# Performance work log

Measured on AMD Instinct MI355X. Metric: run time of the kernel, lower is better.

## Reference

```python
import jax, jax.numpy as jnp
import numpy as np

D = 12            # number of features
N = 1024          # batch size
S = 2 ** D - 1    # number of nonempty subsets (bitmasks 1..2^D-1)
K = 32            # k_neighbors
C = 10            # num_classes
TEMP = 0.5        # temperature
LN_EPS = 1e-5


def _inclusion_matrix():
    # incl[A, B] = 1 if subset B is contained in subset A (bitmask test)
    m = np.arange(1, 2 ** D, dtype=np.int64)
    return ((m[:, None] & m[None, :]) == m[None, :]).astype(np.float32)  # [S, S]

_INCL = _inclusion_matrix()


def setup_inputs() -> dict:
    key = jax.random.key(0)
    ks = jax.random.split(key, 16)
    def g(k, shape, scale):
        return jax.random.normal(k, shape, dtype=jnp.float32) * scale
    return {
        "X": jax.random.normal(ks[0], (N, D), dtype=jnp.float32),
        "y": jax.random.randint(ks[1], (N,), 0, C),
        "enc_w1": g(ks[2], (32, D), 0.3),
        "enc_b1": jnp.zeros((32,), jnp.float32),
        "enc_w2": g(ks[3], (16, 32), 0.2),
        "enc_b2": jnp.zeros((16,), jnp.float32),
        "ln_g": jnp.ones((16,), jnp.float32),
        "ln_b": jnp.zeros((16,), jnp.float32),
        "enc_w3": g(ks[4], (16, 16), 0.25),
        "enc_b3": jnp.zeros((16,), jnp.float32),
        "cap_w1": g(ks[5], (16, 16), 0.1),   # xavier-ish gain=0.1
        "cap_b1": jnp.zeros((16,), jnp.float32),
        "cap_w2": g(ks[6], (S, 16), 0.02),
        "cap_b2": jnp.zeros((S,), jnp.float32),
    }


def _forward(X, y, enc_w1, enc_b1, enc_w2, enc_b2, ln_g, ln_b, enc_w3, enc_b3,
             cap_w1, cap_b1, cap_w2, cap_b2):
    # --- FeatureEncoder (dropout = identity at eval) ---
    h = jax.nn.relu(X @ enc_w1.T + enc_b1)            # [N, 32]
    h = jax.nn.relu(h @ enc_w2.T + enc_b2)            # [N, 16]
    mu = jnp.mean(h, axis=-1, keepdims=True)
    var = jnp.mean((h - mu) ** 2, axis=-1, keepdims=True)
    h = (h - mu) * jax.lax.rsqrt(var + LN_EPS) * ln_g + ln_b
    h = h @ enc_w3.T + enc_b3                         # [N, 16]
    latent = jnp.mean(h, axis=0)                      # [16]

    # --- CapacityGenerator ---
    hc = jax.nn.relu(latent @ cap_w1.T + cap_b1)      # [16]
    increments = jax.nn.sigmoid(hc @ cap_w2.T + cap_b2) * 0.1  # [S]

    # --- compute_capacities_improved: monotone capacities normalized to mu(full)=1 ---
    incl = jnp.asarray(_INCL)                         # [S, S]
    caps = incl @ increments                          # [S]
    caps = caps / (caps[-1] + 1e-8)                   # full set is bitmask 2^D-1 (last)
    cap_lookup = jnp.concatenate([jnp.zeros((1,), caps.dtype), caps])  # index by bitmask, mu(empty)=0

    # --- choquet_similarity_batch for all pairs ---
    s = jnp.exp(-jnp.abs(X[:, None, :] - X[None, :, :]))  # [N, N, D] per-feature sims in (0,1]
    order = jnp.argsort(s, axis=-1)                        # ascending
    vals = jnp.take_along_axis(s, order, axis=-1)          # [N, N, D]
    powers = jnp.left_shift(jnp.int32(1), order.astype(jnp.int32))
    tail = jnp.cumsum(powers[..., ::-1], axis=-1)[..., ::-1]  # bitmask of {sigma(j..D-1)}
    cap = cap_lookup[tail]                                 # [N, N, D]
    prev = jnp.concatenate([jnp.zeros_like(vals[..., :1]), vals[..., :-1]], axis=-1)
    sims = jnp.sum((vals - prev) * cap, axis=-1)           # [N, N] Choquet integral

    # --- leave-one-out top-k softmax vote ---
    sims = sims - jnp.eye(N, dtype=sims.dtype) * 1e9       # exclude self
    top_sims, top_idx = jax.lax.top_k(sims, K)             # [N, K]
    weights = jax.nn.softmax(top_sims / TEMP, axis=-1)     # [N, K]
    labels_k = y[top_idx]                                  # [N, K]
    votes = jnp.einsum('nk,nkc->nc', weights, jax.nn.one_hot(labels_k, C, dtype=weights.dtype))
    return votes, caps


def reference(X, y, enc_w1, enc_b1, enc_w2, enc_b2, ln_g, ln_b, enc_w3, enc_b3,
              cap_w1, cap_b1, cap_w2, cap_b2):
    return _forward(X, y, enc_w1, enc_b1, enc_w2, enc_b2, ln_g, ln_b, enc_w3, enc_b3,
                    cap_w1, cap_b1, cap_w2, cap_b2)
```

## Files before the change

kernel.cpp:

```cpp
#include <hip/hip_runtime.h>

#define ND 12
#define NN 1024
#define NS 4095
#define NK 32
#define NC 10


__global__ __launch_bounds__(64) void k_enc(
    const float* __restrict__ X,
    const float* __restrict__ w1, const float* __restrict__ b1,
    const float* __restrict__ w2, const float* __restrict__ b2,
    const float* __restrict__ lng, const float* __restrict__ lnb,
    const float* __restrict__ w3, const float* __restrict__ b3,
    float* __restrict__ part)
{
    int lane = threadIdx.x;
    int row  = blockIdx.x * 64 + lane;

    float x[ND];
    #pragma unroll
    for (int d = 0; d < ND; ++d) x[d] = X[row * ND + d];

    float h1[32];
    #pragma unroll
    for (int o = 0; o < 32; ++o) {
        float a = b1[o];
        #pragma unroll
        for (int d = 0; d < ND; ++d) a += w1[o * ND + d] * x[d];
        h1[o] = fmaxf(a, 0.f);
    }

    float h2[16];
    #pragma unroll
    for (int o = 0; o < 16; ++o) {
        float a = b2[o];
        #pragma unroll
        for (int k = 0; k < 32; ++k) a += w2[o * 32 + k] * h1[k];
        h2[o] = fmaxf(a, 0.f);
    }

    float mu = 0.f;
    #pragma unroll
    for (int o = 0; o < 16; ++o) mu += h2[o];
    mu *= (1.f / 16.f);
    float var = 0.f;
    #pragma unroll
    for (int o = 0; o < 16; ++o) { float t = h2[o] - mu; var += t * t; }
    var *= (1.f / 16.f);
    float inv = 1.f / sqrtf(var + 1e-5f);

    float hn[16];
    #pragma unroll
    for (int o = 0; o < 16; ++o) hn[o] = (h2[o] - mu) * inv * lng[o] + lnb[o];

    #pragma unroll
    for (int o = 0; o < 16; ++o) {
        float a = b3[o];
        #pragma unroll
        for (int k = 0; k < 16; ++k) a += w3[o * 16 + k] * hn[k];
        #pragma unroll
        for (int s = 1; s < 64; s <<= 1) a += __shfl_xor(a, s, 64);
        if (lane == 0) part[blockIdx.x * 16 + o] = a;
    }
}

__global__ __launch_bounds__(256) void k_inc(
    const float* __restrict__ part,
    const float* __restrict__ cw1, const float* __restrict__ cb1,
    const float* __restrict__ cw2, const float* __restrict__ cb2,
    float* __restrict__ inc)
{
    __shared__ float lat_s[16];
    __shared__ float hc_s[16];
    int tid = threadIdx.x;

    if (tid < 16) {
        float a = 0.f;
        #pragma unroll
        for (int b = 0; b < 16; ++b) a += part[b * 16 + tid];
        lat_s[tid] = a * (1.f / 1024.f);
    }
    __syncthreads();
    if (tid < 16) {
        float a = cb1[tid];
        #pragma unroll
        for (int k = 0; k < 16; ++k) a += cw1[tid * 16 + k] * lat_s[k];
        hc_s[tid] = fmaxf(a, 0.f);
    }
    __syncthreads();

    int e = blockIdx.x * 1024 + tid * 4;
    int s = e >> 4;
    if (s < NS) {
        float4 w = *reinterpret_cast<const float4*>(cw2 + e);
        int k0 = e & 15;
        float p = w.x * hc_s[k0] + w.y * hc_s[k0 + 1] + w.z * hc_s[k0 + 2] + w.w * hc_s[k0 + 3];
        p += __shfl_xor(p, 1, 64);
        p += __shfl_xor(p, 2, 64);
        if ((tid & 3) == 0) {
            float a = p + cb2[s];
            inc[s + 1] = 0.1f / (1.f + __expf(-a));
        }
    }
    if (blockIdx.x == 0 && tid == 0) inc[0] = 0.f;
}

__global__ __launch_bounds__(1024) void k_zeta(
    const float* __restrict__ inc, float* __restrict__ cap_ws, float* __restrict__ out)
{
    __shared__ float arr[4096];
    int tid = threadIdx.x;

    *reinterpret_cast<float4*>(arr + tid * 4) = *reinterpret_cast<const float4*>(inc + tid * 4);
    __syncthreads();

    #pragma unroll 1
    for (int d = 0; d < ND; ++d) {
        int bit = 1 << d;
        #pragma unroll
        for (int r = 0; r < 2; ++r) {
            int i   = tid + r * 1024;
            int low = i & (bit - 1);
            int m   = ((i >> d) << (d + 1)) | bit | low;
            arr[m] += arr[m ^ bit];
        }
        __syncthreads();
    }

    float inv = 1.f / (arr[4095] + 1e-8f);
    #pragma unroll
    for (int r = 0; r < 4; ++r) {
        int m = tid * 4 + r;
        cap_ws[m] = arr[m];
        if (m >= 1) out[NN * NC + m - 1] = arr[m] * inv;
    }
}

#define CSWAP(a,b) { float va=v[a], vb=v[b]; bool sw = va > vb; \
                     v[a]=sw?vb:va; v[b]=sw?va:vb; \
                     int ba=bm[a], bb=bm[b]; bm[a]=sw?bb:ba; bm[b]=sw?ba:bb; }

__global__ __launch_bounds__(256) void k_simsel(
    const float* __restrict__ X, const int* __restrict__ y,
    const float* __restrict__ cap_ws, float* __restrict__ out)
{
    __shared__ float    cap[4096];
    __shared__ unsigned bins[2048];
    __shared__ unsigned wt_u[4];
    __shared__ unsigned ctl_bin, ctl_need;
    __shared__ unsigned vmax_u[4];
    __shared__ float    wsum_s[4];
    __shared__ float    fbins[NC];

    int tid = threadIdx.x, i = blockIdx.x;
    int wv = tid >> 6, ln = tid & 63;

    #pragma unroll
    for (int t = 0; t < 16; ++t) cap[tid + 256 * t] = cap_ws[tid + 256 * t];

    float xi[ND];
    #pragma unroll
    for (int d = 0; d < ND; ++d) xi[d] = X[i * ND + d];
    float inv = 1.f / (cap_ws[4095] + 1e-8f);
    __syncthreads();

    unsigned long long kreg[4];
    #pragma unroll
    for (int t = 0; t < 4; ++t) {
        int j = t * 256 + tid;
        float v[ND]; int bm[ND];
        #pragma unroll
        for (int d = 0; d < ND; ++d) {
            v[d]  = __expf(-fabsf(xi[d] - X[j * ND + d]));
            bm[d] = 1 << d;
        }
        CSWAP(0,1)  CSWAP(0,2)  CSWAP(1,2)  CSWAP(3,4)  CSWAP(3,5)  CSWAP(4,5)
        CSWAP(0,3)  CSWAP(2,5)  CSWAP(2,3)  CSWAP(1,4)  CSWAP(1,2)  CSWAP(3,4)
        CSWAP(6,7)  CSWAP(6,8)  CSWAP(7,8)  CSWAP(9,10) CSWAP(9,11) CSWAP(10,11)
        CSWAP(6,9)  CSWAP(8,11) CSWAP(8,9)  CSWAP(7,10) CSWAP(7,8)  CSWAP(9,10)
        CSWAP(0,6)  CSWAP(4,10) CSWAP(4,6)  CSWAP(2,8)  CSWAP(2,4)  CSWAP(6,8)
        CSWAP(1,7)  CSWAP(5,11) CSWAP(5,7)  CSWAP(3,9)  CSWAP(3,5)  CSWAP(7,9)
        CSWAP(1,2)  CSWAP(3,4)  CSWAP(5,6)  CSWAP(7,8)  CSWAP(9,10)

        int tail = 0; float sim = 0.f;
        #pragma unroll
        for (int k = ND - 1; k >= 0; --k) {
            tail |= bm[k];
            float pv = (k > 0) ? v[k - 1] : 0.f;
            sim += (v[k] - pv) * cap[tail];
        }
        sim *= inv;

        unsigned u = __float_as_uint(sim);
        u = (u & 0x80000000u) ? ~u : (u | 0x80000000u);
        if (j == i) u = 0u;
        kreg[t] = (((unsigned long long)u) << 10) | (unsigned)(1023 - j);
    }

    unsigned mv = 0;
    #pragma unroll
    for (int t = 0; t < 4; ++t) {
        unsigned x = (unsigned)(kreg[t] >> 10);
        mv = (x > mv) ? x : mv;
    }
    #pragma unroll
    for (int s = 1; s < 64; s <<= 1) {
        unsigned o = __shfl_xor(mv, s, 64);
        mv = (o > mv) ? o : mv;
    }
    if (ln == 0) vmax_u[wv] = mv;

    unsigned long long prefix = 0;
    unsigned need = NK;
    #pragma unroll 1
    for (int lev = 0; lev < 4; ++lev) {
        int shift   = (lev < 3) ? (31 - 11 * lev) : 0;
        int bits    = (lev < 3) ? 11 : 9;
        int topbits = shift + bits;
        unsigned mask = (1u << bits) - 1u;

        #pragma unroll
        for (int r = 0; r < 8; ++r) bins[tid + 256 * r] = 0u;
        __syncthreads();

        #pragma unroll
        for (int t = 0; t < 4; ++t) {
            unsigned long long k = kreg[t];
            if ((k >> topbits) == prefix)
                atomicAdd(&bins[(unsigned)(k >> shift) & mask], 1u);
        }
        __syncthreads();

        unsigned s8[8]; unsigned S = 0;
        int base = tid * 8;
        #pragma unroll
        for (int r = 0; r < 8; ++r) { s8[r] = bins[base + r]; S += s8[r]; }
        unsigned v = S;
        #pragma unroll
        for (int off = 1; off < 64; off <<= 1) {
            unsigned o = __shfl_down(v, off, 64);
            if (ln + off < 64) v += o;
        }
        if (ln == 0) wt_u[wv] = v;
        __syncthreads();
        unsigned G = v - S;
        #pragma unroll
        for (int w2 = 0; w2 < 4; ++w2) if (w2 > wv) G += wt_u[w2];

        unsigned cum = G;
        #pragma unroll
        for (int r = 7; r >= 0; --r) {
            unsigned c = s8[r];
            if (cum < need && cum + c >= need) { ctl_bin = (unsigned)(base + r); ctl_need = need - cum; }
            cum += c;
        }
        __syncthreads();
        prefix = (prefix << bits) | ctl_bin;
        need   = ctl_need;
        __syncthreads();
    }
    unsigned long long T = prefix;

    unsigned m0 = vmax_u[0], m1 = vmax_u[1], m2 = vmax_u[2], m3 = vmax_u[3];
    mv = (m1 > m0) ? m1 : m0;
    mv = (m2 > mv) ? m2 : mv;
    mv = (m3 > mv) ? m3 : mv;
    float vmax = (mv & 0x80000000u) ? __uint_as_float(mv & 0x7fffffffu) : __uint_as_float(~mv);

    float wr[4]; float wpart = 0.f;
    #pragma unroll
    for (int t = 0; t < 4; ++t) {
        bool sel = kreg[t] >= T;
        unsigned su = (unsigned)(kreg[t] >> 10);
        float val = (su & 0x80000000u) ? __uint_as_float(su & 0x7fffffffu) : __uint_as_float(~su);
        float w = __expf((val - vmax) * 2.0f);
        w = sel ? w : 0.f;
        wr[t] = w; wpart += w;
    }
    #pragma unroll
    for (int s = 1; s < 64; s <<= 1) wpart += __shfl_xor(wpart, s, 64);
    if (ln == 0) wsum_s[wv] = wpart;
    if (tid < NC) fbins[tid] = 0.f;
    __syncthreads();
    float wsum = wsum_s[0] + wsum_s[1] + wsum_s[2] + wsum_s[3];
    #pragma unroll
    for (int t = 0; t < 4; ++t)
        if (wr[t] != 0.f) atomicAdd(&fbins[y[t * 256 + tid]], wr[t]);
    __syncthreads();
    if (tid < NC) out[i * NC + tid] = fbins[tid] / wsum;
}

extern "C" void kernel_launch(void* const* d_in, const int* in_sizes, int n_in,
                              void* d_out, int out_size, void* d_ws, size_t ws_size,
                              hipStream_t stream)
{
    const float* X   = (const float*)d_in[0];
    const int*   y   = (const int*)  d_in[1];
    const float* w1  = (const float*)d_in[2];
    const float* b1  = (const float*)d_in[3];
    const float* w2  = (const float*)d_in[4];
    const float* b2  = (const float*)d_in[5];
    const float* lng = (const float*)d_in[6];
    const float* lnb = (const float*)d_in[7];
    const float* w3  = (const float*)d_in[8];
    const float* b3  = (const float*)d_in[9];
    const float* cw1 = (const float*)d_in[10];
    const float* cb1 = (const float*)d_in[11];
    const float* cw2 = (const float*)d_in[12];
    const float* cb2 = (const float*)d_in[13];
    float* out = (float*)d_out;
    float* ws  = (float*)d_ws;

    float* cap_ws = ws;
    float* part   = ws + 4096;
    float* inc    = ws + 8192;

    k_enc   <<<16,   64,   0, stream>>>(X, w1, b1, w2, b2, lng, lnb, w3, b3, part);
    k_inc   <<<64,   256,  0, stream>>>(part, cw1, cb1, cw2, cb2, inc);
    k_zeta  <<<1,    1024, 0, stream>>>(inc, cap_ws, out);
    k_simsel<<<NN,   256,  0, stream>>>(X, y, cap_ws, out);
}
```

Baseline: 126.6 us.

## Fuse encoder, capacity generator and zeta transform into one single-block kernel

Merges the three small prep kernels (encoder, increment generator, subset-sum zeta transform) into one 512-thread single-block kernel that keeps partial sums and increments in shared memory, removing two launches and the global round-trips through workspace. The simsel kernel also switches to float4 loads for the cap table, its own row of X and neighbour rows, and clears the histogram bins with uint4 stores. In exchange, the encoder and increment work now run in a single block instead of spread across 16 and 64 blocks, which may lengthen that serial stage.

```diff
diff --git a/kernel.cpp b/kernel.cpp
--- a/kernel.cpp
+++ b/kernel.cpp
@@ -7,78 +7,85 @@
 #define NC 10
 
 
-__global__ __launch_bounds__(64) void k_enc(
+__global__ __launch_bounds__(512) void k_prep(
     const float* __restrict__ X,
     const float* __restrict__ w1, const float* __restrict__ b1,
     const float* __restrict__ w2, const float* __restrict__ b2,
     const float* __restrict__ lng, const float* __restrict__ lnb,
     const float* __restrict__ w3, const float* __restrict__ b3,
-    float* __restrict__ part)
-{
-    int lane = threadIdx.x;
-    int row  = blockIdx.x * 64 + lane;
-
-    float x[ND];
-    #pragma unroll
-    for (int d = 0; d < ND; ++d) x[d] = X[row * ND + d];
-
-    float h1[32];
-    #pragma unroll
-    for (int o = 0; o < 32; ++o) {
-        float a = b1[o];
-        #pragma unroll
-        for (int d = 0; d < ND; ++d) a += w1[o * ND + d] * x[d];
-        h1[o] = fmaxf(a, 0.f);
-    }
-
-    float h2[16];
-    #pragma unroll
-    for (int o = 0; o < 16; ++o) {
-        float a = b2[o];
-        #pragma unroll
-        for (int k = 0; k < 32; ++k) a += w2[o * 32 + k] * h1[k];
-        h2[o] = fmaxf(a, 0.f);
-    }
-
-    float mu = 0.f;
-    #pragma unroll
-    for (int o = 0; o < 16; ++o) mu += h2[o];
-    mu *= (1.f / 16.f);
-    float var = 0.f;
-    #pragma unroll
-    for (int o = 0; o < 16; ++o) { float t = h2[o] - mu; var += t * t; }
-    var *= (1.f / 16.f);
-    float inv = 1.f / sqrtf(var + 1e-5f);
-
-    float hn[16];
-    #pragma unroll
-    for (int o = 0; o < 16; ++o) hn[o] = (h2[o] - mu) * inv * lng[o] + lnb[o];
-
-    #pragma unroll
-    for (int o = 0; o < 16; ++o) {
-        float a = b3[o];
-        #pragma unroll
-        for (int k = 0; k < 16; ++k) a += w3[o * 16 + k] * hn[k];
-        #pragma unroll
-        for (int s = 1; s < 64; s <<= 1) a += __shfl_xor(a, s, 64);
-        if (lane == 0) part[blockIdx.x * 16 + o] = a;
-    }
-}
-
-__global__ __launch_bounds__(256) void k_inc(
-    const float* __restrict__ part,
     const float* __restrict__ cw1, const float* __restrict__ cb1,
     const float* __restrict__ cw2, const float* __restrict__ cb2,
-    float* __restrict__ inc)
+    float* __restrict__ cap_ws, float* __restrict__ out)
 {
+    __shared__ float arr[4096];
+    __shared__ float part[8 * 16];
     __shared__ float lat_s[16];
     __shared__ float hc_s[16];
+
     int tid = threadIdx.x;
+    int wv = tid >> 6, ln = tid & 63;
+
+    float acc[16];
+    #pragma unroll
+    for (int o = 0; o < 16; ++o) acc[o] = 0.f;
+
+    #pragma unroll 1
+    for (int rep = 0; rep < 2; ++rep) {
+        int row = rep * 512 + tid;
+        float x[ND];
+        #pragma unroll
+        for (int d = 0; d < ND; ++d) x[d] = X[row * ND + d];
+
+        float h1[32];
+        #pragma unroll
+        for (int o = 0; o < 32; ++o) {
+            float a = b1[o];
+            #pragma unroll
+            for (int d = 0; d < ND; ++d) a += w1[o * ND + d] * x[d];
+            h1[o] = fmaxf(a, 0.f);
+        }
+        float h2[16];
+        #pragma unroll
+        for (int o = 0; o < 16; ++o) {
+            float a = b2[o];
+            #pragma unroll
+            for (int k = 0; k < 32; ++k) a += w2[o * 32 + k] * h1[k];
+            h2[o] = fmaxf(a, 0.f);
+        }
+        float mu = 0.f;
+        #pragma unroll
+        for (int o = 0; o < 16; ++o) mu += h2[o];
+        mu *= (1.f / 16.f);
+        float var = 0.f;
+        #pragma unroll
+        for (int o = 0; o < 16; ++o) { float t = h2[o] - mu; var += t * t; }
+        var *= (1.f / 16.f);
+        float inv = 1.f / sqrtf(var + 1e-5f);
+        float hn[16];
+        #pragma unroll
+        for (int o = 0; o < 16; ++o) hn[o] = (h2[o] - mu) * inv * lng[o] + lnb[o];
+        #pragma unroll
+        for (int o = 0; o < 16; ++o) {
+            float a = b3[o];
+            #pragma unroll
+            for (int k = 0; k < 16; ++k) a += w3[o * 16 + k] * hn[k];
+            acc[o] += a;
+        }
+    }
+
+    #pragma unroll
+    for (int o = 0; o < 16; ++o) {
+        float a = acc[o];
+        #pragma unroll
+        for (int s = 1; s < 64; s <<= 1) a += __shfl_xor(a, s, 64);
+        if (ln == 0) part[wv * 16 + o] = a;
+    }
+    __syncthreads();
 
     if (tid < 16) {
         float a = 0.f;
         #pragma unroll
-        for (int b = 0; b < 16; ++b) a += part[b * 16 + tid];
+        for (int w = 0; w < 8; ++w) a += part[w * 16 + tid];
         lat_s[tid] = a * (1.f / 1024.f);
     }
     __syncthreads();
@@ -90,37 +97,33 @@
     }
     __syncthreads();
 
-    int e = blockIdx.x * 1024 + tid * 4;
-    int s = e >> 4;
-    if (s < NS) {
-        float4 w = *reinterpret_cast<const float4*>(cw2 + e);
-        int k0 = e & 15;
-        float p = w.x * hc_s[k0] + w.y * hc_s[k0 + 1] + w.z * hc_s[k0 + 2] + w.w * hc_s[k0 + 3];
-        p += __shfl_xor(p, 1, 64);
-        p += __shfl_xor(p, 2, 64);
-        if ((tid & 3) == 0) {
-            float a = p + cb2[s];
-            inc[s + 1] = 0.1f / (1.f + __expf(-a));
-        }
-    }
-    if (blockIdx.x == 0 && tid == 0) inc[0] = 0.f;
-}
-
-__global__ __launch_bounds__(1024) void k_zeta(
-    const float* __restrict__ inc, float* __restrict__ cap_ws, float* __restrict__ out)
-{
-    __shared__ float arr[4096];
-    int tid = threadIdx.x;
-
-    *reinterpret_cast<float4*>(arr + tid * 4) = *reinterpret_cast<const float4*>(inc + tid * 4);
+    float hc[16];
+    #pragma unroll
+    for (int k = 0; k < 16; ++k) hc[k] = hc_s[k];
+    const float4* cw24 = reinterpret_cast<const float4*>(cw2);
+    #pragma unroll 1
+    for (int r = 0; r < 8; ++r) {
+        int s = tid + r * 512;
+        if (s < NS) {
+            float4 wa = cw24[s * 4 + 0], wb = cw24[s * 4 + 1];
+            float4 wc = cw24[s * 4 + 2], wd = cw24[s * 4 + 3];
+            float a = cb2[s]
+                + wa.x * hc[0]  + wa.y * hc[1]  + wa.z * hc[2]  + wa.w * hc[3]
+                + wb.x * hc[4]  + wb.y * hc[5]  + wb.z * hc[6]  + wb.w * hc[7]
+                + wc.x * hc[8]  + wc.y * hc[9]  + wc.z * hc[10] + wc.w * hc[11]
+                + wd.x * hc[12] + wd.y * hc[13] + wd.z * hc[14] + wd.w * hc[15];
+            arr[s + 1] = 0.1f / (1.f + __expf(-a));
+        }
+    }
+    if (tid == 0) arr[0] = 0.f;
     __syncthreads();
 
     #pragma unroll 1
     for (int d = 0; d < ND; ++d) {
         int bit = 1 << d;
         #pragma unroll
-        for (int r = 0; r < 2; ++r) {
-            int i   = tid + r * 1024;
+        for (int r = 0; r < 4; ++r) {
+            int i   = tid + r * 512;
             int low = i & (bit - 1);
             int m   = ((i >> d) << (d + 1)) | bit | low;
             arr[m] += arr[m ^ bit];
@@ -130,10 +133,11 @@
 
     float inv = 1.f / (arr[4095] + 1e-8f);
     #pragma unroll
-    for (int r = 0; r < 4; ++r) {
-        int m = tid * 4 + r;
-        cap_ws[m] = arr[m];
-        if (m >= 1) out[NN * NC + m - 1] = arr[m] * inv;
+    for (int r = 0; r < 8; ++r) {
+        int m = tid + r * 512;
+        float c = arr[m];
+        cap_ws[m] = c;
+        if (m >= 1) out[NN * NC + m - 1] = c * inv;
     }
 }
 
@@ -156,12 +160,19 @@
     int tid = threadIdx.x, i = blockIdx.x;
     int wv = tid >> 6, ln = tid & 63;
 
-    #pragma unroll
-    for (int t = 0; t < 16; ++t) cap[tid + 256 * t] = cap_ws[tid + 256 * t];
-
+    const float4* cap4 = reinterpret_cast<const float4*>(cap_ws);
+    #pragma unroll
+    for (int t = 0; t < 4; ++t)
+        reinterpret_cast<float4*>(cap)[tid + 256 * t] = cap4[tid + 256 * t];
+
+    const float4* X4 = reinterpret_cast<const float4*>(X);
     float xi[ND];
-    #pragma unroll
-    for (int d = 0; d < ND; ++d) xi[d] = X[i * ND + d];
+    {
+        float4 a = X4[i * 3], b = X4[i * 3 + 1], c = X4[i * 3 + 2];
+        xi[0]=a.x; xi[1]=a.y; xi[2]=a.z; xi[3]=a.w;
+        xi[4]=b.x; xi[5]=b.y; xi[6]=b.z; xi[7]=b.w;
+        xi[8]=c.x; xi[9]=c.y; xi[10]=c.z; xi[11]=c.w;
+    }
     float inv = 1.f / (cap_ws[4095] + 1e-8f);
     __syncthreads();
 
@@ -169,10 +180,17 @@
     #pragma unroll
     for (int t = 0; t < 4; ++t) {
         int j = t * 256 + tid;
+        float xr[ND];
+        {
+            float4 a = X4[j * 3], b = X4[j * 3 + 1], c = X4[j * 3 + 2];
+            xr[0]=a.x; xr[1]=a.y; xr[2]=a.z; xr[3]=a.w;
+            xr[4]=b.x; xr[5]=b.y; xr[6]=b.z; xr[7]=b.w;
+            xr[8]=c.x; xr[9]=c.y; xr[10]=c.z; xr[11]=c.w;
+        }
         float v[ND]; int bm[ND];
         #pragma unroll
         for (int d = 0; d < ND; ++d) {
-            v[d]  = __expf(-fabsf(xi[d] - X[j * ND + d]));
+            v[d]  = __expf(-fabsf(xi[d] - xr[d]));
             bm[d] = 1 << d;
         }
         CSWAP(0,1)  CSWAP(0,2)  CSWAP(1,2)  CSWAP(3,4)  CSWAP(3,5)  CSWAP(4,5)
@@ -220,8 +238,9 @@
         int topbits = shift + bits;
         unsigned mask = (1u << bits) - 1u;
 
-        #pragma unroll
-        for (int r = 0; r < 8; ++r) bins[tid + 256 * r] = 0u;
+        uint4 z; z.x = z.y = z.z = z.w = 0u;
+        reinterpret_cast<uint4*>(bins)[tid * 2]     = z;
+        reinterpret_cast<uint4*>(bins)[tid * 2 + 1] = z;
         __syncthreads();
 
         #pragma unroll
@@ -313,11 +332,8 @@
     float* ws  = (float*)d_ws;
 
     float* cap_ws = ws;
-    float* part   = ws + 4096;
-    float* inc    = ws + 8192;
-
-    k_enc   <<<16,   64,   0, stream>>>(X, w1, b1, w2, b2, lng, lnb, w3, b3, part);
-    k_inc   <<<64,   256,  0, stream>>>(part, cw1, cb1, cw2, cb2, inc);
-    k_zeta  <<<1,    1024, 0, stream>>>(inc, cap_ws, out);
-    k_simsel<<<NN,   256,  0, stream>>>(X, y, cap_ws, out);
+
+    k_prep  <<<1,  512, 0, stream>>>(X, w1, b1, w2, b2, lng, lnb, w3, b3,
+                                     cw1, cb1, cw2, cb2, cap_ws, out);
+    k_simsel<<<NN, 256, 0, stream>>>(X, y, cap_ws, out);
 }
```

Result: slower. 163.3 us (+29.0%).

## Prescale X by log2e, vectorize loads, stage encoder weights in LDS, trim radix-select syncs

Applied to the files above, without the earlier changes.

The encoder kernel now writes a copy of X pre-multiplied by log2(e), so the similarity kernel can use exp2f instead of __expf. Encoder weights are staged in shared memory, and X, cap and bins are read or written with float4/uint4 vector accesses. In the radix select, bins are zeroed right after being read, which removes one barrier per level. The changes target load traffic and per-level synchronisation, at the cost of an extra workspace buffer and a written copy of X.

```diff
diff --git a/kernel.cpp b/kernel.cpp
--- a/kernel.cpp
+++ b/kernel.cpp
@@ -5,41 +5,67 @@
 #define NS 4095
 #define NK 32
 #define NC 10
-
-
-__global__ __launch_bounds__(64) void k_enc(
+#define LOG2E 1.4426950408889634f
+
+
+__global__ __launch_bounds__(128) void k_enc(
     const float* __restrict__ X,
     const float* __restrict__ w1, const float* __restrict__ b1,
     const float* __restrict__ w2, const float* __restrict__ b2,
     const float* __restrict__ lng, const float* __restrict__ lnb,
     const float* __restrict__ w3, const float* __restrict__ b3,
-    float* __restrict__ part)
-{
-    int lane = threadIdx.x;
-    int row  = blockIdx.x * 64 + lane;
-
+    float* __restrict__ part, float* __restrict__ x2)
+{
+    __shared__ float sw[1248];
+    int tid = threadIdx.x;
+    int row = blockIdx.x * 128 + tid;
+    int wv = tid >> 6, ln = tid & 63;
+
+    for (int k = tid; k < 384; k += 128) sw[k] = w1[k];
+    if (tid < 32) sw[384 + tid] = b1[tid];
+    for (int k = tid; k < 512; k += 128) sw[416 + k] = w2[k];
+    if (tid < 16) {
+        sw[928 + tid]  = b2[tid];
+        sw[944 + tid]  = lng[tid];
+        sw[960 + tid]  = lnb[tid];
+        sw[1232 + tid] = b3[tid];
+    }
+    for (int k = tid; k < 256; k += 128) sw[976 + k] = w3[k];
+
+    const float4* X4 = reinterpret_cast<const float4*>(X);
     float x[ND];
-    #pragma unroll
-    for (int d = 0; d < ND; ++d) x[d] = X[row * ND + d];
+    {
+        float4 a = X4[row * 3], b = X4[row * 3 + 1], c = X4[row * 3 + 2];
+        x[0]=a.x; x[1]=a.y; x[2]=a.z; x[3]=a.w;
+        x[4]=b.x; x[5]=b.y; x[6]=b.z; x[7]=b.w;
+        x[8]=c.x; x[9]=c.y; x[10]=c.z; x[11]=c.w;
+    }
+    {
+        float4 a, b, c;
+        a.x=x[0]*LOG2E; a.y=x[1]*LOG2E; a.z=x[2]*LOG2E;  a.w=x[3]*LOG2E;
+        b.x=x[4]*LOG2E; b.y=x[5]*LOG2E; b.z=x[6]*LOG2E;  b.w=x[7]*LOG2E;
+        c.x=x[8]*LOG2E; c.y=x[9]*LOG2E; c.z=x[10]*LOG2E; c.w=x[11]*LOG2E;
+        float4* x24 = reinterpret_cast<float4*>(x2);
+        x24[row * 3] = a; x24[row * 3 + 1] = b; x24[row * 3 + 2] = c;
+    }
+    __syncthreads();
 
     float h1[32];
     #pragma unroll
     for (int o = 0; o < 32; ++o) {
-        float a = b1[o];
-        #pragma unroll
-        for (int d = 0; d < ND; ++d) a += w1[o * ND + d] * x[d];
+        float a = sw[384 + o];
+        #pragma unroll
+        for (int d = 0; d < ND; ++d) a += sw[o * ND + d] * x[d];
         h1[o] = fmaxf(a, 0.f);
     }
-
     float h2[16];
     #pragma unroll
     for (int o = 0; o < 16; ++o) {
-        float a = b2[o];
-        #pragma unroll
-        for (int k = 0; k < 32; ++k) a += w2[o * 32 + k] * h1[k];
+        float a = sw[928 + o];
+        #pragma unroll
+        for (int k = 0; k < 32; ++k) a += sw[416 + o * 32 + k] * h1[k];
         h2[o] = fmaxf(a, 0.f);
     }
-
     float mu = 0.f;
     #pragma unroll
     for (int o = 0; o < 16; ++o) mu += h2[o];
@@ -49,19 +75,18 @@
     for (int o = 0; o < 16; ++o) { float t = h2[o] - mu; var += t * t; }
     var *= (1.f / 16.f);
     float inv = 1.f / sqrtf(var + 1e-5f);
-
     float hn[16];
     #pragma unroll
-    for (int o = 0; o < 16; ++o) hn[o] = (h2[o] - mu) * inv * lng[o] + lnb[o];
+    for (int o = 0; o < 16; ++o) hn[o] = (h2[o] - mu) * inv * sw[944 + o] + sw[960 + o];
 
     #pragma unroll
     for (int o = 0; o < 16; ++o) {
-        float a = b3[o];
-        #pragma unroll
-        for (int k = 0; k < 16; ++k) a += w3[o * 16 + k] * hn[k];
+        float a = sw[1232 + o];
+        #pragma unroll
+        for (int k = 0; k < 16; ++k) a += sw[976 + o * 16 + k] * hn[k];
         #pragma unroll
         for (int s = 1; s < 64; s <<= 1) a += __shfl_xor(a, s, 64);
-        if (lane == 0) part[blockIdx.x * 16 + o] = a;
+        if (ln == 0) part[(blockIdx.x * 2 + wv) * 16 + o] = a;
     }
 }
 
@@ -142,7 +167,7 @@
                      int ba=bm[a], bb=bm[b]; bm[a]=sw?bb:ba; bm[b]=sw?ba:bb; }
 
 __global__ __launch_bounds__(256) void k_simsel(
-    const float* __restrict__ X, const int* __restrict__ y,
+    const float* __restrict__ x2, const int* __restrict__ y,
     const float* __restrict__ cap_ws, float* __restrict__ out)
 {
     __shared__ float    cap[4096];
@@ -156,12 +181,26 @@
     int tid = threadIdx.x, i = blockIdx.x;
     int wv = tid >> 6, ln = tid & 63;
 
-    #pragma unroll
-    for (int t = 0; t < 16; ++t) cap[tid + 256 * t] = cap_ws[tid + 256 * t];
-
+    const float4* cap4 = reinterpret_cast<const float4*>(cap_ws);
+    #pragma unroll
+    for (int t = 0; t < 4; ++t)
+        reinterpret_cast<float4*>(cap)[tid + 256 * t] = cap4[tid + 256 * t];
+
+    {
+        uint4 z; z.x = z.y = z.z = z.w = 0u;
+        reinterpret_cast<uint4*>(bins)[tid * 2]     = z;
+        reinterpret_cast<uint4*>(bins)[tid * 2 + 1] = z;
+    }
+    if (tid < NC) fbins[tid] = 0.f;
+
+    const float4* X4 = reinterpret_cast<const float4*>(x2);
     float xi[ND];
-    #pragma unroll
-    for (int d = 0; d < ND; ++d) xi[d] = X[i * ND + d];
+    {
+        float4 a = X4[i * 3], b = X4[i * 3 + 1], c = X4[i * 3 + 2];
+        xi[0]=a.x; xi[1]=a.y; xi[2]=a.z; xi[3]=a.w;
+        xi[4]=b.x; xi[5]=b.y; xi[6]=b.z; xi[7]=b.w;
+        xi[8]=c.x; xi[9]=c.y; xi[10]=c.z; xi[11]=c.w;
+    }
     float inv = 1.f / (cap_ws[4095] + 1e-8f);
     __syncthreads();
 
@@ -169,10 +208,17 @@
     #pragma unroll
     for (int t = 0; t < 4; ++t) {
         int j = t * 256 + tid;
+        float xr[ND];
+        {
+            float4 a = X4[j * 3], b = X4[j * 3 + 1], c = X4[j * 3 + 2];
+            xr[0]=a.x; xr[1]=a.y; xr[2]=a.z; xr[3]=a.w;
+            xr[4]=b.x; xr[5]=b.y; xr[6]=b.z; xr[7]=b.w;
+            xr[8]=c.x; xr[9]=c.y; xr[10]=c.z; xr[11]=c.w;
+        }
         float v[ND]; int bm[ND];
         #pragma unroll
         for (int d = 0; d < ND; ++d) {
-            v[d]  = __expf(-fabsf(xi[d] - X[j * ND + d]));
+            v[d]  = exp2f(-fabsf(xi[d] - xr[d]));
             bm[d] = 1 << d;
         }
         CSWAP(0,1)  CSWAP(0,2)  CSWAP(1,2)  CSWAP(3,4)  CSWAP(3,5)  CSWAP(4,5)
@@ -221,10 +267,6 @@
         unsigned mask = (1u << bits) - 1u;
 
         #pragma unroll
-        for (int r = 0; r < 8; ++r) bins[tid + 256 * r] = 0u;
-        __syncthreads();
-
-        #pragma unroll
         for (int t = 0; t < 4; ++t) {
             unsigned long long k = kreg[t];
             if ((k >> topbits) == prefix)
@@ -236,6 +278,11 @@
         int base = tid * 8;
         #pragma unroll
         for (int r = 0; r < 8; ++r) { s8[r] = bins[base + r]; S += s8[r]; }
+        {
+            uint4 z; z.x = z.y = z.z = z.w = 0u;
+            reinterpret_cast<uint4*>(bins)[tid * 2]     = z;
+            reinterpret_cast<uint4*>(bins)[tid * 2 + 1] = z;
+        }
         unsigned v = S;
         #pragma unroll
         for (int off = 1; off < 64; off <<= 1) {
@@ -258,7 +305,6 @@
         __syncthreads();
         prefix = (prefix << bits) | ctl_bin;
         need   = ctl_need;
-        __syncthreads();
     }
     unsigned long long T = prefix;
 
@@ -281,7 +327,6 @@
     #pragma unroll
     for (int s = 1; s < 64; s <<= 1) wpart += __shfl_xor(wpart, s, 64);
     if (ln == 0) wsum_s[wv] = wpart;
-    if (tid < NC) fbins[tid] = 0.f;
     __syncthreads();
     float wsum = wsum_s[0] + wsum_s[1] + wsum_s[2] + wsum_s[3];
     #pragma unroll
@@ -315,9 +360,10 @@
     float* cap_ws = ws;
     float* part   = ws + 4096;
     float* inc    = ws + 8192;
-
-    k_enc   <<<16,   64,   0, stream>>>(X, w1, b1, w2, b2, lng, lnb, w3, b3, part);
-    k_inc   <<<64,   256,  0, stream>>>(part, cw1, cb1, cw2, cb2, inc);
-    k_zeta  <<<1,    1024, 0, stream>>>(inc, cap_ws, out);
-    k_simsel<<<NN,   256,  0, stream>>>(X, y, cap_ws, out);
-}
+    float* x2     = ws + 16384;
+
+    k_enc   <<<8,  128,  0, stream>>>(X, w1, b1, w2, b2, lng, lnb, w3, b3, part, x2);
+    k_inc   <<<64, 256,  0, stream>>>(part, cw1, cb1, cw2, cb2, inc);
+    k_zeta  <<<1,  1024, 0, stream>>>(inc, cap_ws, out);
+    k_simsel<<<NN, 256,  0, stream>>>(x2, y, cap_ws, out);
+}
```

Measured after the change: 119.6 us. -5.5%, faster.
